# Optimization experiments

Hardware: AMD Instinct MI355X
Metric: run time of the kernel (lower is better)

The kernel has to match this reference:

```python
import jax, jax.numpy as jnp
from jax import lax
import numpy as np

B, S, D, H2, V = 1024, 256, 128, 5, 50257
EPS = 1e-5


def setup_inputs() -> dict:
    key = jax.random.key(0)
    ks = jax.random.split(key, 12)
    s = 0.08  # init scale ~ 1/sqrt(D)
    return {
        "x": jax.random.randint(ks[0], (B, S), 0, V),
        "emb": jax.random.normal(ks[1], (V, D), jnp.float32) * s,
        "W_ih1": jax.random.normal(ks[2], (D, D), jnp.float32) * s,
        "b_ih1": jax.random.normal(ks[3], (D,), jnp.float32) * s,
        "W_hh1": jax.random.normal(ks[4], (D, D), jnp.float32) * s,
        "b_hh1": jax.random.normal(ks[5], (D,), jnp.float32) * s,
        "g1": jnp.ones((D,), jnp.float32),
        "be1": jnp.zeros((D,), jnp.float32),
        "W_ih2": jax.random.normal(ks[6], (H2, D), jnp.float32) * s,
        "b_ih2": jax.random.normal(ks[7], (H2,), jnp.float32) * s,
        "W_hh2": jax.random.normal(ks[8], (H2, H2), jnp.float32) * s,
        "b_hh2": jax.random.normal(ks[9], (H2,), jnp.float32) * s,
        "g2": jnp.ones((H2,), jnp.float32),
        "be2": jnp.zeros((H2,), jnp.float32),
    }


def _rnn(xproj, W_hh):
    """Vanilla tanh RNN. xproj: [B,S,H] = x @ W_ih^T + b_ih + b_hh (precomputed)."""
    h0 = jnp.zeros((xproj.shape[0], W_hh.shape[0]), xproj.dtype)

    def step(h, xt):  # xt: [B,H]
        h = jnp.tanh(xt + h @ W_hh.T)
        return h, h

    _, hs = lax.scan(step, h0, jnp.swapaxes(xproj, 0, 1))  # [S,B,H]
    return jnp.swapaxes(hs, 0, 1)  # [B,S,H]


def _ln(z, g, b):
    m = jnp.mean(z, axis=-1, keepdims=True)
    v = jnp.mean(jnp.square(z - m), axis=-1, keepdims=True)
    return (z - m) * lax.rsqrt(v + EPS) * g + b


def reference(x, emb, W_ih1, b_ih1, W_hh1, b_hh1, g1, be1,
              W_ih2, b_ih2, W_hh2, b_hh2, g2, be2):
    e = emb[x]  # [B,S,D]
    z = _rnn(e @ W_ih1.T + (b_ih1 + b_hh1), W_hh1)
    z = _ln(z, g1, be1)
    z = _rnn(z @ W_ih2.T + (b_ih2 + b_hh2), W_hh2)  # [B,S,5]
    z = _ln(z, g2, be2)
    pooled = jnp.mean(z, axis=1)  # AvgPool1d over full seq -> [B,5]
    return jax.nn.softmax(pooled, axis=1)
```

## Files before the change

kernel.cpp:

```cpp
#include <hip/hip_runtime.h>
#include <stdint.h>

#define S_LEN 256
#define DIM   128
#define EPSL  1e-5f

typedef __bf16 bf16x8 __attribute__((ext_vector_type(8)));
typedef float  f32x4  __attribute__((ext_vector_type(4)));

__device__ __forceinline__ unsigned short f2bf_bits(float f) {
  union { float f; unsigned int u; } v; v.f = f;
  unsigned int r = v.u + 0x7fffu + ((v.u >> 16) & 1u);
  return (unsigned short)(r >> 16);
}
__device__ __forceinline__ float bf2f_bits(unsigned short b) {
  union { float f; unsigned int u; } v; v.u = ((unsigned int)b) << 16; return v.f;
}
__device__ __forceinline__ unsigned f2bf_rhu(float f) {
  return (__float_as_uint(f) + 0x8000u) >> 16;
}
__device__ __forceinline__ unsigned pack_rhu(float lo, float hi) {
  return __builtin_amdgcn_perm(__float_as_uint(hi) + 0x8000u,
                               __float_as_uint(lo) + 0x8000u, 0x07060302u);
}
__device__ __forceinline__ float tanh_fast(float x) {
  float e = __expf(2.f * x);
  return 1.f - 2.f * __builtin_amdgcn_rcpf(e + 1.f);
}

template<int CTRL>
__device__ __forceinline__ float dpp_rot_add(float v) {
  int r = __builtin_amdgcn_update_dpp(0, __float_as_int(v), CTRL, 0xF, 0xF, true);
  return v + __int_as_float(r);
}
template<int CTRL>
__device__ __forceinline__ float dpp_rot_max(float v) {
  int r = __builtin_amdgcn_update_dpp(0, __float_as_int(v), CTRL, 0xF, 0xF, true);
  return fmaxf(v, __int_as_float(r));
}
__device__ __forceinline__ float dpp_sum16(float v) {
  v = dpp_rot_add<0x124>(v); v = dpp_rot_add<0x128>(v);
  v = dpp_rot_add<0x39>(v);  v = dpp_rot_add<0x4E>(v);
  return v;
}
__device__ __forceinline__ float dpp_max16(float v) {
  v = dpp_rot_max<0x124>(v); v = dpp_rot_max<0x128>(v);
  v = dpp_rot_max<0x39>(v);  v = dpp_rot_max<0x4E>(v);
  return v;
}
template<int CTRL>
__device__ __forceinline__ void red_level7(float& s, float& sq, float* d) {
  s  = dpp_rot_add<CTRL>(s);
  sq = dpp_rot_add<CTRL>(sq);
#pragma unroll
  for (int j = 0; j < 5; j++) d[j] = dpp_rot_add<CTRL>(d[j]);
}
template<int JJ>
__device__ __forceinline__ float bcast16(float v) {
  int r = __builtin_amdgcn_ds_swizzle(__float_as_int(v), (JJ << 5) | 0x10);
  return __int_as_float(r);
}

union Frag8 { unsigned short us[8]; bf16x8 v; int4 i4; };

__global__ __launch_bounds__(512, 2)
void rnn_fused(const int* __restrict__ x, const float* __restrict__ emb,
               const float* __restrict__ Wih1, const float* __restrict__ bih1,
               const float* __restrict__ Whh1, const float* __restrict__ bhh1,
               const float* __restrict__ g1, const float* __restrict__ be1,
               const float* __restrict__ Wih2, const float* __restrict__ bih2,
               const float* __restrict__ Whh2, const float* __restrict__ bhh2,
               const float* __restrict__ g2, const float* __restrict__ be2,
               float* __restrict__ out)
{
  __shared__ __align__(16) unsigned short h_bf[2][16 * 128];
  __shared__ __align__(16) unsigned short e_bf[2][16 * 128];
  __shared__ int x_tile[16 * 256];

  const int tid  = threadIdx.x;
  const int wave = tid >> 6;
  const int lane = tid & 63;
  const int r0   = blockIdx.x * 16;
  const int l15  = lane & 15;
  const int q    = lane >> 4;

  for (int i = tid; i < 16 * 256; i += 512)
    x_tile[i] = x[(size_t)(r0 + (i >> 8)) * S_LEN + (i & 255)];
  for (int i = tid; i < 16 * 128; i += 512) h_bf[1][i] = 0;

  const int n1 = wave * 16 + l15;
  const float bias1v = bih1[n1] + bhh1[n1];
  bf16x8 whi[4], wlo[4], wih[4];
#pragma unroll
  for (int kt = 0; kt < 4; kt++) {
    int k0 = kt * 32 + q * 8;
    Frag8 fh, fl, fa;
#pragma unroll
    for (int j = 0; j < 8; j++) {
      float w = Whh1[n1 * DIM + k0 + j];
      unsigned short hi = f2bf_bits(w);
      fh.us[j] = hi;
      fl.us[j] = f2bf_bits(w - bf2f_bits(hi));
      fa.us[j] = f2bf_bits(Wih1[n1 * DIM + k0 + j]);
    }
    whi[kt] = fh.v; wlo[kt] = fl.v; wih[kt] = fa.v;
  }

  const bool ln_role = (wave < 4);
  float w2g[5][8], Gs[5], Bs[5], wrow[5];
  float t2_l = 0.f, g2_l = 0.f, be2_l = 0.f, validf = 0.f;
  float h2rep[5], pool_l = 0.f;
  int myrow = 0;
  float pf[2][8];
  const int gm   = (wave & 3) * 4 + q;
  const int goct = l15;
  const int gdst = gm * 128 + ((goct ^ gm) & 15) * 8;

  if (ln_role) {
    myrow = wave * 4 + q;
    int coct = (l15 ^ myrow) & 15;
#pragma unroll
    for (int j = 0; j < 8; j++) {
      int c = coct * 8 + j;
      float gc = g1[c];
#pragma unroll
      for (int jj = 0; jj < 5; jj++) w2g[jj][j] = Wih2[jj * DIM + c] * gc;
    }
#pragma unroll
    for (int jj = 0; jj < 5; jj++) { Gs[jj] = 0.f; Bs[jj] = 0.f; }
    for (int c = 0; c < DIM; c++) {
      float gc = g1[c], bc = be1[c];
#pragma unroll
      for (int jj = 0; jj < 5; jj++) {
        float w = Wih2[jj * DIM + c];
        Gs[jj] += w * gc; Bs[jj] += w * bc;
      }
    }
    validf = (l15 < 5) ? 1.f : 0.f;
    if (l15 < 5) {
      t2_l = bih2[l15] + bhh2[l15];
      g2_l = g2[l15]; be2_l = be2[l15];
#pragma unroll
      for (int jj = 0; jj < 5; jj++) wrow[jj] = Whh2[l15 * 5 + jj];
    } else {
#pragma unroll
      for (int jj = 0; jj < 5; jj++) wrow[jj] = 0.f;
    }
#pragma unroll
    for (int jj = 0; jj < 5; jj++) h2rep[jj] = 0.f;
  }
  __syncthreads();

  if (!ln_role) {
    float ta[8], tb[8];
    { int xid = x_tile[gm * 256 + 0];
      const float* pe = emb + (size_t)xid * DIM + goct * 8;
#pragma unroll
      for (int j = 0; j < 8; j++) ta[j] = pe[j]; }
    { int xid = x_tile[gm * 256 + 1];
      const float* pe = emb + (size_t)xid * DIM + goct * 8;
#pragma unroll
      for (int j = 0; j < 8; j++) tb[j] = pe[j]; }
    { int xid = x_tile[gm * 256 + 2];
      const float* pe = emb + (size_t)xid * DIM + goct * 8;
#pragma unroll
      for (int j = 0; j < 8; j++) pf[0][j] = pe[j]; }
    { int xid = x_tile[gm * 256 + 3];
      const float* pe = emb + (size_t)xid * DIM + goct * 8;
#pragma unroll
      for (int j = 0; j < 8; j++) pf[1][j] = pe[j]; }
    Frag8 pa, pb;
#pragma unroll
    for (int j = 0; j < 8; j++) { pa.us[j] = f2bf_bits(ta[j]); pb.us[j] = f2bf_bits(tb[j]); }
    *(int4*)&e_bf[0][gdst] = pa.i4;
    *(int4*)&e_bf[1][gdst] = pb.i4;
  }
  __syncthreads();

  f32x4 xpacc = {bias1v, bias1v, bias1v, bias1v};
#pragma unroll
  for (int kt = 0; kt < 4; kt++) {
    int sw = (((kt * 4 + q) ^ l15) & 15) * 8;
    bf16x8 ae = *(const bf16x8*)&e_bf[0][l15 * 128 + sw];
    xpacc = __builtin_amdgcn_mfma_f32_16x16x32_bf16(ae, wih[kt], xpacc, 0, 0, 0);
  }
  asm volatile("s_waitcnt lgkmcnt(0)\n\ts_barrier" ::: "memory");

#pragma unroll 2
  for (int t = 0; t <= S_LEN; t++) {
    Frag8 hr;
    const bool do_ln = ln_role && (t >= 1) && (t <= S_LEN);
    if (do_ln)
      hr.i4 = *(const int4*)&h_bf[(t - 1) & 1][myrow * 128 + l15 * 8];

    asm volatile("s_setprio 1" :::);
    f32x4 ah_a = {0.f, 0.f, 0.f, 0.f}, ah_b = {0.f, 0.f, 0.f, 0.f};
    f32x4 al_a = xpacc,                 al_b = {0.f, 0.f, 0.f, 0.f};
    if (t < S_LEN) {
      const int rb = (t + 1) & 1;
#pragma unroll
      for (int kt = 0; kt < 4; kt++) {
        int sw = (((kt * 4 + q) ^ l15) & 15) * 8;
        bf16x8 ahf = *(const bf16x8*)&h_bf[rb][l15 * 128 + sw];
        if (kt < 2) {
          ah_a = __builtin_amdgcn_mfma_f32_16x16x32_bf16(ahf, whi[kt], ah_a, 0, 0, 0);
          al_a = __builtin_amdgcn_mfma_f32_16x16x32_bf16(ahf, wlo[kt], al_a, 0, 0, 0);
        } else {
          ah_b = __builtin_amdgcn_mfma_f32_16x16x32_bf16(ahf, whi[kt], ah_b, 0, 0, 0);
          al_b = __builtin_amdgcn_mfma_f32_16x16x32_bf16(ahf, wlo[kt], al_b, 0, 0, 0);
        }
      }
      const int wb = t & 1;
      const int c = n1;
      const int oct = c >> 3;
#pragma unroll
      for (int r = 0; r < 4; r++) {
        int row = q * 4 + r;
        float av = (ah_a[r] + al_a[r]) + (ah_b[r] + al_b[r]);
        h_bf[wb][row * 128 + ((oct ^ row) & 15) * 8 + (c & 7)] =
            (unsigned short)f2bf_rhu(tanh_fast(av));
      }
    }
    asm volatile("s_setprio 0" :::);

    if (t + 1 < S_LEN) {
      f32x4 ea = {bias1v, bias1v, bias1v, bias1v};
      f32x4 eb = {0.f, 0.f, 0.f, 0.f};
#pragma unroll
      for (int kt = 0; kt < 4; kt++) {
        int sw = (((kt * 4 + q) ^ l15) & 15) * 8;
        bf16x8 ae = *(const bf16x8*)&e_bf[(t + 1) & 1][l15 * 128 + sw];
        if (kt < 2)
          ea = __builtin_amdgcn_mfma_f32_16x16x32_bf16(ae, wih[kt], ea, 0, 0, 0);
        else
          eb = __builtin_amdgcn_mfma_f32_16x16x32_bf16(ae, wih[kt], eb, 0, 0, 0);
      }
#pragma unroll
      for (int r = 0; r < 4; r++) xpacc[r] = ea[r] + eb[r];
    }

    if (!ln_role) {
      if (t + 2 < S_LEN) {
        int4 pk;
        pk.x = pack_rhu(pf[t & 1][0], pf[t & 1][1]);
        pk.y = pack_rhu(pf[t & 1][2], pf[t & 1][3]);
        pk.z = pack_rhu(pf[t & 1][4], pf[t & 1][5]);
        pk.w = pack_rhu(pf[t & 1][6], pf[t & 1][7]);
        *(int4*)&e_bf[t & 1][gdst] = pk;
      }
      if (t + 4 < S_LEN) {
        int xid = x_tile[gm * 256 + t + 4];
        const float* pe = emb + (size_t)xid * DIM + goct * 8;
#pragma unroll
        for (int j = 0; j < 8; j++) pf[t & 1][j] = pe[j];
      }
    } else if (do_ln) {
      float s = 0.f, sq = 0.f, d[5] = {0, 0, 0, 0, 0};
#pragma unroll
      for (int j = 0; j < 8; j++) {
        float v = bf2f_bits(hr.us[j]);
        s += v; sq += v * v;
#pragma unroll
        for (int jj = 0; jj < 5; jj++) d[jj] = fmaf(w2g[jj][j], v, d[jj]);
      }
      red_level7<0x124>(s, sq, d);
      red_level7<0x128>(s, sq, d);
      red_level7<0x39>(s, sq, d);
      red_level7<0x4E>(s, sq, d);
      float mean = s * (1.f / 128.f);
      float var  = sq * (1.f / 128.f) - mean * mean;
      float rstd = rsqrtf(var + EPSL);
      float p[5];
#pragma unroll
      for (int jj = 0; jj < 5; jj++)
        p[jj] = rstd * (d[jj] - mean * Gs[jj]) + Bs[jj];
      float psel = (l15 == 0) ? p[0] : (l15 == 1) ? p[1] :
                   (l15 == 2) ? p[2] : (l15 == 3) ? p[3] : p[4];
      float a = psel + t2_l;
#pragma unroll
      for (int jj = 0; jj < 5; jj++) a = fmaf(wrow[jj], h2rep[jj], a);
      float xn = tanh_fast(a);
      float s2 = dpp_sum16(xn * validf) * 0.2f;
      float dd = xn - s2;
      float v2 = dpp_sum16(dd * dd * validf) * 0.2f;
      float r2 = rsqrtf(v2 + EPSL);
      pool_l += dd * r2 * g2_l + be2_l;
      h2rep[0] = bcast16<0>(xn); h2rep[1] = bcast16<1>(xn);
      h2rep[2] = bcast16<2>(xn); h2rep[3] = bcast16<3>(xn);
      h2rep[4] = bcast16<4>(xn);
    }
    asm volatile("s_waitcnt lgkmcnt(0)\n\ts_barrier" ::: "memory");
  }

  if (ln_role) {
    float lg = pool_l * (1.f / 256.f);
    float mx = dpp_max16((l15 < 5) ? lg : -3.0e38f);
    float e  = (l15 < 5) ? __expf(lg - mx) : 0.f;
    float sm = dpp_sum16(e);
    if (l15 < 5) out[(size_t)(r0 + myrow) * 5 + l15] = e / sm;
  }
}

extern "C" void kernel_launch(void* const* d_in, const int* in_sizes, int n_in,
                              void* d_out, int out_size, void* d_ws, size_t ws_size,
                              hipStream_t stream) {
  (void)in_sizes; (void)n_in; (void)d_ws; (void)ws_size; (void)out_size;
  rnn_fused<<<dim3(64), dim3(512), 0, stream>>>(
      (const int*)  d_in[0],  (const float*)d_in[1],  (const float*)d_in[2],
      (const float*)d_in[3],  (const float*)d_in[4],  (const float*)d_in[5],
      (const float*)d_in[6],  (const float*)d_in[7],  (const float*)d_in[8],
      (const float*)d_in[9],  (const float*)d_in[10], (const float*)d_in[11],
      (const float*)d_in[12], (const float*)d_in[13], (float*)d_out);
}
```

Before: 316.2 us.

## Drop split-bf16 W_hh precision and serialize MFMA accumulation chains

Replaces the hi/lo split-bf16 representation of W_hh1 with a single bf16 copy, halving the MFMAs on the serial recurrence critical path. The dual accumulator chains are collapsed into one dependent chain for both the hidden and input projections. The s_setprio hints are removed, and the LayerNorm hidden-state load moves from the top of the step to just before its use. This reduces per-step latency but loses the extra precision of the recurrent matmul, so error can accumulate over 256 steps.

```diff
diff --git a/kernel.cpp b/kernel.cpp
--- a/kernel.cpp
+++ b/kernel.cpp
@@ -90,20 +90,17 @@
 
   const int n1 = wave * 16 + l15;
   const float bias1v = bih1[n1] + bhh1[n1];
-  bf16x8 whi[4], wlo[4], wih[4];
+  bf16x8 wh[4], wih[4];
 #pragma unroll
   for (int kt = 0; kt < 4; kt++) {
     int k0 = kt * 32 + q * 8;
-    Frag8 fh, fl, fa;
+    Frag8 fh, fa;
 #pragma unroll
     for (int j = 0; j < 8; j++) {
-      float w = Whh1[n1 * DIM + k0 + j];
-      unsigned short hi = f2bf_bits(w);
-      fh.us[j] = hi;
-      fl.us[j] = f2bf_bits(w - bf2f_bits(hi));
+      fh.us[j] = f2bf_bits(Whh1[n1 * DIM + k0 + j]);
       fa.us[j] = f2bf_bits(Wih1[n1 * DIM + k0 + j]);
     }
-    whi[kt] = fh.v; wlo[kt] = fl.v; wih[kt] = fa.v;
+    wh[kt] = fh.v; wih[kt] = fa.v;
   }
 
   const bool ln_role = (wave < 4);
@@ -188,27 +185,14 @@
 
 #pragma unroll 2
   for (int t = 0; t <= S_LEN; t++) {
-    Frag8 hr;
-    const bool do_ln = ln_role && (t >= 1) && (t <= S_LEN);
-    if (do_ln)
-      hr.i4 = *(const int4*)&h_bf[(t - 1) & 1][myrow * 128 + l15 * 8];
-
-    asm volatile("s_setprio 1" :::);
-    f32x4 ah_a = {0.f, 0.f, 0.f, 0.f}, ah_b = {0.f, 0.f, 0.f, 0.f};
-    f32x4 al_a = xpacc,                 al_b = {0.f, 0.f, 0.f, 0.f};
+    f32x4 acc = xpacc;
     if (t < S_LEN) {
       const int rb = (t + 1) & 1;
 #pragma unroll
       for (int kt = 0; kt < 4; kt++) {
         int sw = (((kt * 4 + q) ^ l15) & 15) * 8;
         bf16x8 ahf = *(const bf16x8*)&h_bf[rb][l15 * 128 + sw];
-        if (kt < 2) {
-          ah_a = __builtin_amdgcn_mfma_f32_16x16x32_bf16(ahf, whi[kt], ah_a, 0, 0, 0);
-          al_a = __builtin_amdgcn_mfma_f32_16x16x32_bf16(ahf, wlo[kt], al_a, 0, 0, 0);
-        } else {
-          ah_b = __builtin_amdgcn_mfma_f32_16x16x32_bf16(ahf, whi[kt], ah_b, 0, 0, 0);
-          al_b = __builtin_amdgcn_mfma_f32_16x16x32_bf16(ahf, wlo[kt], al_b, 0, 0, 0);
-        }
+        acc = __builtin_amdgcn_mfma_f32_16x16x32_bf16(ahf, wh[kt], acc, 0, 0, 0);
       }
       const int wb = t & 1;
       const int c = n1;
@@ -216,27 +200,20 @@
 #pragma unroll
       for (int r = 0; r < 4; r++) {
         int row = q * 4 + r;
-        float av = (ah_a[r] + al_a[r]) + (ah_b[r] + al_b[r]);
         h_bf[wb][row * 128 + ((oct ^ row) & 15) * 8 + (c & 7)] =
-            (unsigned short)f2bf_rhu(tanh_fast(av));
-      }
-    }
-    asm volatile("s_setprio 0" :::);
+            (unsigned short)f2bf_rhu(tanh_fast(acc[r]));
+      }
+    }
 
     if (t + 1 < S_LEN) {
-      f32x4 ea = {bias1v, bias1v, bias1v, bias1v};
-      f32x4 eb = {0.f, 0.f, 0.f, 0.f};
+      f32x4 a = {bias1v, bias1v, bias1v, bias1v};
 #pragma unroll
       for (int kt = 0; kt < 4; kt++) {
         int sw = (((kt * 4 + q) ^ l15) & 15) * 8;
         bf16x8 ae = *(const bf16x8*)&e_bf[(t + 1) & 1][l15 * 128 + sw];
-        if (kt < 2)
-          ea = __builtin_amdgcn_mfma_f32_16x16x32_bf16(ae, wih[kt], ea, 0, 0, 0);
-        else
-          eb = __builtin_amdgcn_mfma_f32_16x16x32_bf16(ae, wih[kt], eb, 0, 0, 0);
-      }
-#pragma unroll
-      for (int r = 0; r < 4; r++) xpacc[r] = ea[r] + eb[r];
+        a = __builtin_amdgcn_mfma_f32_16x16x32_bf16(ae, wih[kt], a, 0, 0, 0);
+      }
+      xpacc = a;
     }
 
     if (!ln_role) {
@@ -254,7 +231,10 @@
 #pragma unroll
         for (int j = 0; j < 8; j++) pf[t & 1][j] = pe[j];
       }
-    } else if (do_ln) {
+    } else if (t >= 1) {
+      const int hb = (t - 1) & 1;
+      Frag8 hr;
+      hr.i4 = *(const int4*)&h_bf[hb][myrow * 128 + l15 * 8];
       float s = 0.f, sq = 0.f, d[5] = {0, 0, 0, 0, 0};
 #pragma unroll
       for (int j = 0; j < 8; j++) {
```

Result: faster. 281.3 us (-11.0%).
